# Performance work log

Measured on AMD Instinct MI355X. Metric: run time of the kernel, lower is better.

Reference implementation:

```python
import jax, jax.numpy as jnp
import numpy as np

DIM = 2048
INTER = 1408
N_EXPERTS = 16
TOP_K = 2
N_SHARED = 2
SHARED_INTER = N_SHARED * INTER  # 2816


def setup_inputs() -> dict:
    key = jax.random.key(0)
    ks = jax.random.split(key, 9)
    s = 0.02
    return {
        "x": jax.random.normal(ks[0], (4, 2048, DIM), dtype=jnp.float32),
        "gate_w": jax.random.normal(ks[1], (N_EXPERTS, DIM), dtype=jnp.float32) * s,
        "w1": jax.random.normal(ks[2], (N_EXPERTS, INTER, DIM), dtype=jnp.float32) * s,
        "w2": jax.random.normal(ks[3], (N_EXPERTS, DIM, INTER), dtype=jnp.float32) * s,
        "w3": jax.random.normal(ks[4], (N_EXPERTS, INTER, DIM), dtype=jnp.float32) * s,
        "sw1": jax.random.normal(ks[5], (SHARED_INTER, DIM), dtype=jnp.float32) * s,
        "sw2": jax.random.normal(ks[6], (DIM, SHARED_INTER), dtype=jnp.float32) * s,
        "sw3": jax.random.normal(ks[7], (SHARED_INTER, DIM), dtype=jnp.float32) * s,
    }


def _swiglu(t, wa, wb, wo):
    # t: [T, d_in]; wa, wb: [d_h, d_in]; wo: [d_out, d_h]
    h = jax.nn.silu(t @ wa.T) * (t @ wb.T)
    return h @ wo.T


def reference(x, gate_w, w1, w2, w3, sw1, sw2, sw3):
    shape = x.shape
    t = x.reshape(-1, DIM)                      # [T, dim]
    scores = jax.nn.softmax(t @ gate_w.T, axis=-1)  # [T, E]
    weights, indices = jax.lax.top_k(scores, TOP_K)  # [T, k] each

    y = jnp.zeros_like(t)
    # Small fixed loop over experts (structurally distinct weights).
    # Per-token combine weight for expert e: sum over top-k slots routed to e
    # (matches y[idx] += expert(x[idx]) * weights[idx, top]; zero weight for
    # unrouted tokens reproduces the counts[i]==0 skip exactly).
    for e in range(N_EXPERTS):
        w_e = jnp.sum(jnp.where(indices == e, weights, 0.0), axis=-1)  # [T]
        y = y + _swiglu(t, w1[e], w3[e], w2[e]) * w_e[:, None]

    z = _swiglu(t, sw1, sw3, sw2)               # shared experts MLP
    return (y + z).reshape(shape)
```

## Files before the change

### kernel.cpp

```cpp
#include <hip/hip_runtime.h>
#include <hip/hip_bf16.h>

#define DIM 2048
#define INTER 1408
#define NEXP 16
#define NTOK 8192
#define SINTER 2816

typedef __attribute__((ext_vector_type(8))) short bf16x8;
typedef __attribute__((ext_vector_type(4))) float f32x4;
typedef __attribute__((ext_vector_type(4))) unsigned short u16x4;
typedef __attribute__((ext_vector_type(8))) unsigned short u16x8;

#define VMCNT(n) asm volatile("s_waitcnt vmcnt(" #n ")" ::: "memory")
#define BARRIER() __builtin_amdgcn_s_barrier()

__device__ __forceinline__ unsigned short f2bf(float f) {
    union { float f; unsigned u; } a; a.f = f;
    unsigned r = a.u + 0x7fffu + ((a.u >> 16) & 1u);
    return (unsigned short)(r >> 16);
}
__device__ __forceinline__ float bf2f(unsigned short u) {
    union { unsigned u; float f; } a; a.u = ((unsigned)u) << 16; return a.f;
}

__device__ __forceinline__ void gload16(const void* g, void* lds) {
    __builtin_amdgcn_global_load_lds(
        (const __attribute__((address_space(1))) void*)g,
        (__attribute__((address_space(3))) void*)lds, 16, 0, 0);
}

__global__ __launch_bounds__(256) void cast_bf16(const float* __restrict__ s,
                                                 unsigned short* __restrict__ d,
                                                 long long n) {
    long long i = ((long long)blockIdx.x * 256 + threadIdx.x) * 8;
    if (i >= n) return;
    float4 a = *(const float4*)(s + i), b = *(const float4*)(s + i + 4);
    u16x8 o = { f2bf(a.x), f2bf(a.y), f2bf(a.z), f2bf(a.w),
                f2bf(b.x), f2bf(b.y), f2bf(b.z), f2bf(b.w) };
    *(u16x8*)(d + i) = o;
}

__global__ __launch_bounds__(256) void gate_topk(
    const float* __restrict__ x, const float* __restrict__ gw,
    unsigned short* __restrict__ xb,
    int* __restrict__ counts, int* __restrict__ toklist,
    int* __restrict__ se, int* __restrict__ sp, float* __restrict__ swt) {
    int wave = threadIdx.x >> 6;
    int lane = threadIdx.x & 63;
    int tok  = blockIdx.x * 4 + wave;
    const float* xr = x + (size_t)tok * DIM;
    unsigned short* xbr = xb + (size_t)tok * DIM;

    float part[NEXP];
#pragma unroll
    for (int e = 0; e < NEXP; ++e) part[e] = 0.f;
#pragma unroll
    for (int c = 0; c < DIM / 256; ++c) {
        float4 xv = *(const float4*)(xr + c * 256 + lane * 4);
        u16x4 xo = { f2bf(xv.x), f2bf(xv.y), f2bf(xv.z), f2bf(xv.w) };
        *(u16x4*)(xbr + c * 256 + lane * 4) = xo;
#pragma unroll
        for (int e = 0; e < NEXP; ++e) {
            float4 g = *(const float4*)(gw + e * DIM + c * 256 + lane * 4);
            part[e] += xv.x * g.x + xv.y * g.y + xv.z * g.z + xv.w * g.w;
        }
    }
#pragma unroll
    for (int e = 0; e < NEXP; ++e) {
        float v = part[e];
#pragma unroll
        for (int off = 32; off; off >>= 1) v += __shfl_xor(v, off);
        part[e] = v;
    }
    float mx = part[0];
#pragma unroll
    for (int e = 1; e < NEXP; ++e) mx = fmaxf(mx, part[e]);
    float Z = 0.f;
#pragma unroll
    for (int e = 0; e < NEXP; ++e) Z += expf(part[e] - mx);
    int i1 = 0; float m1 = part[0];
#pragma unroll
    for (int e = 1; e < NEXP; ++e) if (part[e] > m1) { m1 = part[e]; i1 = e; }
    int i2 = -1; float m2 = -1e30f;
#pragma unroll
    for (int e = 0; e < NEXP; ++e) if (e != i1 && part[e] > m2) { m2 = part[e]; i2 = e; }
    if (lane == 0) {
        float w1v = expf(m1 - mx) / Z;
        float w2v = expf(m2 - mx) / Z;
        int p1 = atomicAdd(&counts[i1], 1);
        toklist[i1 * NTOK + p1] = tok;
        int p2 = atomicAdd(&counts[i2], 1);
        toklist[i2 * NTOK + p2] = tok;
        se[2 * tok] = i1;  sp[2 * tok] = p1;  swt[2 * tok] = w1v;
        se[2 * tok + 1] = i2;  sp[2 * tok + 1] = p2;  swt[2 * tok + 1] = w2v;
    }
}

__global__ void prefix_k(const int* __restrict__ counts, int* __restrict__ base) {
    if (threadIdx.x == 0) {
        int acc = 0;
        for (int e = 0; e < NEXP; ++e) { base[e] = acc; acc += counts[e]; }
        base[16] = acc;
        base[17] = acc + NTOK;
    }
}

__global__ __launch_bounds__(512, 2) void gemm1(
    const unsigned short* __restrict__ xb,
    const unsigned short* __restrict__ w1b, const unsigned short* __restrict__ w3b,
    const unsigned short* __restrict__ sw1b, const unsigned short* __restrict__ sw3b,
    const int* __restrict__ counts, const int* __restrict__ base,
    const int* __restrict__ toklist, unsigned short* __restrict__ hbuf) {
    const int e   = blockIdx.z;
    const int cnt = (e < NEXP) ? counts[e] : NTOK;
    const int m0  = blockIdx.y * 256;
    if (m0 >= cnt) return;
    const int n0  = blockIdx.x * 128;
    const size_t woff = (size_t)((e < NEXP) ? e : e - NEXP) * INTER * DIM;
    const unsigned short* B1 = ((e < NEXP) ? w1b : sw1b) + woff;
    const unsigned short* B3 = ((e < NEXP) ? w3b : sw3b) + woff;
    const int hbase = base[e];
    const int* tl = toklist + e * NTOK;

    __shared__ __attribute__((aligned(16))) unsigned short As[2][16384];
    __shared__ __attribute__((aligned(16))) unsigned short B1s[2][8192];
    __shared__ __attribute__((aligned(16))) unsigned short B3s[2][8192];

    const int tid = threadIdx.x;
    const int w = tid >> 6, lu = tid & 63;
    const int wr = w >> 1, wc = w & 1;
    const int lr = lu & 15, hi = lu >> 4;

    const int srow = tid >> 3;
    const int sslot = tid & 7;
    const int cEl = ((sslot ^ (srow & 7)) * 8);

    const unsigned short* aSrc[4];
#pragma unroll
    for (int i = 0; i < 4; ++i) {
        int grow = m0 + 64 * i + srow;
        int t;
        if (e < NEXP) t = (grow < cnt) ? tl[grow] : 0;
        else          t = grow;
        aSrc[i] = xb + (size_t)t * DIM + cEl;
    }
    const unsigned short *b1Src[2], *b3Src[2];
#pragma unroll
    for (int i = 0; i < 2; ++i) {
        int r = n0 + 64 * i + srow;
        b1Src[i] = B1 + (size_t)r * DIM + cEl;
        b3Src[i] = B3 + (size_t)r * DIM + cEl;
    }

    int aoff[2][4], boff[2][4];
#pragma unroll
    for (int kk = 0; kk < 2; ++kk) {
#pragma unroll
        for (int m = 0; m < 4; ++m) {
            int R = wr * 64 + m * 16 + lr;
            aoff[kk][m] = R * 128 + (((kk * 4 + hi) ^ (lr & 7)) << 4);
        }
#pragma unroll
        for (int n = 0; n < 4; ++n) {
            int R = wc * 64 + n * 16 + lr;
            boff[kk][n] = R * 128 + (((kk * 4 + hi) ^ (lr & 7)) << 4);
        }
    }

    f32x4 acc1[4][4], acc3[4][4];
#pragma unroll
    for (int m = 0; m < 4; ++m)
#pragma unroll
        for (int n = 0; n < 4; ++n) {
            acc1[m][n] = (f32x4){0.f, 0.f, 0.f, 0.f};
            acc3[m][n] = (f32x4){0.f, 0.f, 0.f, 0.f};
        }

    const int H = DIM / 64;

    auto STAGE = [&](int hh) {
        int hb = hh & 1;
        int kc = hh * 64;
#pragma unroll
        for (int i = 0; i < 4; ++i)
            gload16(aSrc[i] + kc, &As[hb][i * 4096 + tid * 8]);
#pragma unroll
        for (int i = 0; i < 2; ++i) {
            gload16(b1Src[i] + kc, &B1s[hb][i * 4096 + tid * 8]);
            gload16(b3Src[i] + kc, &B3s[hb][i * 4096 + tid * 8]);
        }
    };

    STAGE(0);
    VMCNT(0);
    BARRIER();

    for (int h = 0; h < H; ++h) {
        const int hb = h & 1;
        const char* As_ = (const char*)&As[hb][0];
        const char* B1_ = (const char*)&B1s[hb][0];
        const char* B3_ = (const char*)&B3s[hb][0];
        bf16x8 af[4], b1f[4], b3f[4];
#pragma unroll
        for (int m = 0; m < 4; ++m) af[m] = *(const bf16x8*)(As_ + aoff[0][m]);
#pragma unroll
        for (int n = 0; n < 4; ++n) {
            b1f[n] = *(const bf16x8*)(B1_ + boff[0][n]);
            b3f[n] = *(const bf16x8*)(B3_ + boff[0][n]);
        }
        if (h + 1 < H) STAGE(h + 1);
        __builtin_amdgcn_s_setprio(1);
#pragma unroll
        for (int n = 0; n < 4; ++n)
#pragma unroll
            for (int m = 0; m < 4; ++m)
                acc1[m][n] = __builtin_amdgcn_mfma_f32_16x16x32_bf16(af[m], b1f[n], acc1[m][n], 0, 0, 0);
#pragma unroll
        for (int n = 0; n < 4; ++n)
#pragma unroll
            for (int m = 0; m < 4; ++m)
                acc3[m][n] = __builtin_amdgcn_mfma_f32_16x16x32_bf16(af[m], b3f[n], acc3[m][n], 0, 0, 0);
        __builtin_amdgcn_s_setprio(0);
#pragma unroll
        for (int m = 0; m < 4; ++m) af[m] = *(const bf16x8*)(As_ + aoff[1][m]);
#pragma unroll
        for (int n = 0; n < 4; ++n) {
            b1f[n] = *(const bf16x8*)(B1_ + boff[1][n]);
            b3f[n] = *(const bf16x8*)(B3_ + boff[1][n]);
        }
        __builtin_amdgcn_s_setprio(1);
#pragma unroll
        for (int n = 0; n < 4; ++n)
#pragma unroll
            for (int m = 0; m < 4; ++m)
                acc1[m][n] = __builtin_amdgcn_mfma_f32_16x16x32_bf16(af[m], b1f[n], acc1[m][n], 0, 0, 0);
#pragma unroll
        for (int n = 0; n < 4; ++n)
#pragma unroll
            for (int m = 0; m < 4; ++m)
                acc3[m][n] = __builtin_amdgcn_mfma_f32_16x16x32_bf16(af[m], b3f[n], acc3[m][n], 0, 0, 0);
        __builtin_amdgcn_s_setprio(0);
        VMCNT(0);
        BARRIER();
    }

#pragma unroll
    for (int m = 0; m < 4; ++m) {
#pragma unroll
        for (int i = 0; i < 4; ++i) {
            int row  = wr * 64 + m * 16 + hi * 4 + i;
            int grow = m0 + row;
            if (grow < cnt) {
                size_t ro = (size_t)(hbase + grow) * INTER;
#pragma unroll
                for (int n = 0; n < 4; ++n) {
                    int col = n0 + wc * 64 + n * 16 + lr;
                    float a = acc1[m][n][i];
                    float hv = a / (1.f + __expf(-a)) * acc3[m][n][i];
                    hbuf[ro + col] = f2bf(hv);
                }
            }
        }
    }
}

__global__ __launch_bounds__(512, 2) void gemm2(
    const unsigned short* __restrict__ hbuf,
    const unsigned short* __restrict__ w2b, const unsigned short* __restrict__ sw2b,
    const int* __restrict__ counts, const int* __restrict__ base,
    unsigned short* __restrict__ g2buf) {
    const int e   = blockIdx.z;
    const int cnt = (e < NEXP) ? counts[e] : NTOK;
    const int m0  = blockIdx.y * 256;
    if (m0 >= cnt) return;
    const int n0  = blockIdx.x * 256;
    const int hbase = base[e];
    const size_t bstride = (e < NEXP) ? INTER : SINTER;
    const unsigned short* Bb = (e < NEXP) ? w2b + (size_t)e * DIM * INTER
                                          : sw2b + (size_t)(e - NEXP) * INTER;

    __shared__ __attribute__((aligned(16))) unsigned short Ah[2][16384];
    __shared__ __attribute__((aligned(16))) unsigned short Bh[2][16384];

    const int tid = threadIdx.x;
    const int w = tid >> 6, lu = tid & 63;
    const int wr = w >> 2, wc = w & 3;
    const int lr = lu & 15, hi = lu >> 4;

    const int srow = tid >> 3;
    const int sslot = tid & 7;
    const int cEl = ((sslot ^ (srow & 7)) * 8);

    const unsigned short* aSrc[4];
#pragma unroll
    for (int i = 0; i < 4; ++i)
        aSrc[i] = hbuf + (size_t)(hbase + m0 + 64 * i + srow) * INTER + cEl;
    const unsigned short* bSrc[4];
#pragma unroll
    for (int i = 0; i < 4; ++i)
        bSrc[i] = Bb + (size_t)(n0 + 64 * i + srow) * bstride + cEl;

    int aoff[2][8], boff[2][4];
#pragma unroll
    for (int kk = 0; kk < 2; ++kk) {
#pragma unroll
        for (int m = 0; m < 8; ++m) {
            int R = wr * 128 + m * 16 + lr;
            aoff[kk][m] = R * 128 + (((kk * 4 + hi) ^ (lr & 7)) << 4);
        }
#pragma unroll
        for (int n = 0; n < 4; ++n) {
            int R = wc * 64 + n * 16 + lr;
            boff[kk][n] = R * 128 + (((kk * 4 + hi) ^ (lr & 7)) << 4);
        }
    }

    f32x4 acc[8][4];
#pragma unroll
    for (int m = 0; m < 8; ++m)
#pragma unroll
        for (int n = 0; n < 4; ++n) acc[m][n] = (f32x4){0.f, 0.f, 0.f, 0.f};

    const int H = INTER / 64;

    auto STAGE = [&](int hh) {
        int hb = hh & 1;
        int kc = hh * 64;
#pragma unroll
        for (int i = 0; i < 4; ++i)
            gload16(aSrc[i] + kc, &Ah[hb][i * 4096 + tid * 8]);
#pragma unroll
        for (int i = 0; i < 4; ++i)
            gload16(bSrc[i] + kc, &Bh[hb][i * 4096 + tid * 8]);
    };

    STAGE(0);
    VMCNT(0);
    BARRIER();

    for (int h = 0; h < H; ++h) {
        const int hb = h & 1;
        const char* A_ = (const char*)&Ah[hb][0];
        const char* B_ = (const char*)&Bh[hb][0];
        bf16x8 af[8], bf[4];
#pragma unroll
        for (int m = 0; m < 8; ++m) af[m] = *(const bf16x8*)(A_ + aoff[0][m]);
#pragma unroll
        for (int n = 0; n < 4; ++n) bf[n] = *(const bf16x8*)(B_ + boff[0][n]);
        if (h + 1 < H) STAGE(h + 1);
        __builtin_amdgcn_s_setprio(1);
#pragma unroll
        for (int n = 0; n < 4; ++n)
#pragma unroll
            for (int m = 0; m < 8; ++m)
                acc[m][n] = __builtin_amdgcn_mfma_f32_16x16x32_bf16(af[m], bf[n], acc[m][n], 0, 0, 0);
        __builtin_amdgcn_s_setprio(0);
#pragma unroll
        for (int m = 0; m < 8; ++m) af[m] = *(const bf16x8*)(A_ + aoff[1][m]);
#pragma unroll
        for (int n = 0; n < 4; ++n) bf[n] = *(const bf16x8*)(B_ + boff[1][n]);
        __builtin_amdgcn_s_setprio(1);
#pragma unroll
        for (int n = 0; n < 4; ++n)
#pragma unroll
            for (int m = 0; m < 8; ++m)
                acc[m][n] = __builtin_amdgcn_mfma_f32_16x16x32_bf16(af[m], bf[n], acc[m][n], 0, 0, 0);
        __builtin_amdgcn_s_setprio(0);
        VMCNT(0);
        BARRIER();
    }

#pragma unroll
    for (int m = 0; m < 8; ++m) {
#pragma unroll
        for (int i = 0; i < 4; ++i) {
            int row  = wr * 128 + m * 16 + hi * 4 + i;
            int grow = m0 + row;
            if (grow < cnt) {
                unsigned short* orow = g2buf + (size_t)(hbase + grow) * DIM + n0 + wc * 64 + lr;
#pragma unroll
                for (int n = 0; n < 4; ++n)
                    orow[n * 16] = f2bf(acc[m][n][i]);
            }
        }
    }
}

__global__ __launch_bounds__(256) void combine(
    const unsigned short* __restrict__ g2buf, const int* __restrict__ base,
    const int* __restrict__ se, const int* __restrict__ sp,
    const float* __restrict__ swt, float* __restrict__ out) {
    const int tok = blockIdx.x;
    const int c = threadIdx.x * 8;
    const int e0 = se[2 * tok], e1 = se[2 * tok + 1];
    const float w0 = swt[2 * tok], w1 = swt[2 * tok + 1];
    const size_t r0 = (size_t)(base[e0] + sp[2 * tok]) * DIM + c;
    const size_t r1 = (size_t)(base[e1] + sp[2 * tok + 1]) * DIM + c;
    const size_t r2 = (size_t)(2 * NTOK + tok) * DIM + c;
    const size_t r3 = (size_t)(3 * NTOK + tok) * DIM + c;
    u16x8 a = *(const u16x8*)(g2buf + r0);
    u16x8 b = *(const u16x8*)(g2buf + r1);
    u16x8 s0 = *(const u16x8*)(g2buf + r2);
    u16x8 s1 = *(const u16x8*)(g2buf + r3);
    float o[8];
#pragma unroll
    for (int j = 0; j < 8; ++j)
        o[j] = w0 * bf2f(a[j]) + w1 * bf2f(b[j]) + bf2f(s0[j]) + bf2f(s1[j]);
    float4* op = (float4*)(out + (size_t)tok * DIM + c);
    op[0] = make_float4(o[0], o[1], o[2], o[3]);
    op[1] = make_float4(o[4], o[5], o[6], o[7]);
}

extern "C" void kernel_launch(void* const* d_in, const int* in_sizes, int n_in,
                              void* d_out, int out_size, void* d_ws, size_t ws_size,
                              hipStream_t stream) {
    const float* x   = (const float*)d_in[0];
    const float* gw  = (const float*)d_in[1];
    const float* w1  = (const float*)d_in[2];
    const float* w2  = (const float*)d_in[3];
    const float* w3  = (const float*)d_in[4];
    const float* sw1 = (const float*)d_in[5];
    const float* sw2 = (const float*)d_in[6];
    const float* sw3 = (const float*)d_in[7];
    float* out = (float*)d_out;

    char* ws = (char*)d_ws;
    int*   counts  = (int*)ws;
    int*   basep   = (int*)(ws + 128);
    int*   toklist = (int*)(ws + 4096);
    int*   se      = (int*)(ws + 4096 + 524288);
    int*   sp      = (int*)(ws + 4096 + 524288 + 65536);
    float* swt     = (float*)(ws + 4096 + 524288 + 131072);

    unsigned short* hbuf = (unsigned short*)(ws + (2u << 20));

    const size_t hbytes = (size_t)4 * NTOK * INTER * 2;
    const size_t offx   = (2ull << 20) + hbytes;
    const size_t xbytes = (size_t)NTOK * DIM * 2;
    const size_t offw   = offx + xbytes;
    const size_t wB     = (size_t)NEXP * INTER * DIM * 2;
    const size_t swB    = (size_t)SINTER * DIM * 2;

    unsigned short* xb   = (unsigned short*)(ws + offx);
    unsigned short* w1b  = (unsigned short*)(ws + offw);
    unsigned short* w3b  = (unsigned short*)(ws + offw + wB);
    unsigned short* w2b  = (unsigned short*)(ws + offw + 2 * wB);
    unsigned short* sw1b = (unsigned short*)(ws + offw + 3 * wB);
    unsigned short* sw3b = (unsigned short*)(ws + offw + 3 * wB + swB);
    unsigned short* sw2b = (unsigned short*)(ws + offw + 3 * wB + 2 * swB);

    unsigned short* g2buf = (unsigned short*)(ws + offx);

    hipMemsetAsync(counts, 0, 64, stream);

    auto cast = [&](const float* s, unsigned short* d, long long n) {
        cast_bf16<<<(int)((n / 8 + 255) / 256), 256, 0, stream>>>(s, d, n);
    };
    cast(w1, w1b, (long long)NEXP * INTER * DIM);
    cast(w3, w3b, (long long)NEXP * INTER * DIM);
    cast(sw1, sw1b, (long long)SINTER * DIM);
    cast(sw3, sw3b, (long long)SINTER * DIM);
    cast(w2, w2b, (long long)NEXP * INTER * DIM);
    cast(sw2, sw2b, (long long)SINTER * DIM);

    gate_topk<<<NTOK / 4, 256, 0, stream>>>(x, gw, xb, counts, toklist, se, sp, swt);
    prefix_k<<<1, 64, 0, stream>>>(counts, basep);

    gemm1<<<dim3(INTER / 128, NTOK / 256, 18), 512, 0, stream>>>(
        xb, w1b, w3b, sw1b, sw3b, counts, basep, toklist, hbuf);

    gemm2<<<dim3(DIM / 256, NTOK / 256, 18), 512, 0, stream>>>(
        hbuf, w2b, sw2b, counts, basep, g2buf);

    combine<<<NTOK, 256, 0, stream>>>(g2buf, basep, se, sp, swt, out);
}
```

Before: 1.187 ms.

## Triple-buffer A tiles in expert GEMMs and fuse weight casts into one launch

Both grouped GEMMs now keep three LDS buffers for the gathered A tile and prefetch A two K-steps ahead (B one step ahead), issuing loads at the top of each iteration and waiting with a partial vmcnt. The aim is to hide the latency of the gathered activation loads behind more MFMA work. The six separate fp32-to-bf16 weight cast launches are merged into one kernel that picks the source by range, cutting launch overhead. The extra A buffer raises LDS use per block (gemm1 to 160KB with two blocks per CU requested), which may reduce occupancy. The partial vmcnt counts also have to match the number of loads actually issued.

```diff
diff --git a/kernel.cpp b/kernel.cpp
--- a/kernel.cpp
+++ b/kernel.cpp
@@ -30,15 +30,28 @@
         (__attribute__((address_space(3))) void*)lds, 16, 0, 0);
 }
 
-__global__ __launch_bounds__(256) void cast_bf16(const float* __restrict__ s,
-                                                 unsigned short* __restrict__ d,
-                                                 long long n) {
+__global__ __launch_bounds__(256) void cast_all(
+    const float* __restrict__ w1, const float* __restrict__ w3,
+    const float* __restrict__ w2, const float* __restrict__ sw1,
+    const float* __restrict__ sw3, const float* __restrict__ sw2,
+    unsigned short* __restrict__ w1b, unsigned short* __restrict__ w3b,
+    unsigned short* __restrict__ w2b, unsigned short* __restrict__ sw1b,
+    unsigned short* __restrict__ sw3b, unsigned short* __restrict__ sw2b) {
+    const long long NW = (long long)NEXP * INTER * DIM;
+    const long long NS = (long long)SINTER * DIM;
     long long i = ((long long)blockIdx.x * 256 + threadIdx.x) * 8;
-    if (i >= n) return;
-    float4 a = *(const float4*)(s + i), b = *(const float4*)(s + i + 4);
+    const float* s; unsigned short* d; long long off;
+    if      (i < NW)            { s = w1;  d = w1b;  off = i; }
+    else if (i < 2 * NW)        { s = w3;  d = w3b;  off = i - NW; }
+    else if (i < 3 * NW)        { s = w2;  d = w2b;  off = i - 2 * NW; }
+    else if (i < 3 * NW + NS)   { s = sw1; d = sw1b; off = i - 3 * NW; }
+    else if (i < 3 * NW + 2*NS) { s = sw3; d = sw3b; off = i - 3 * NW - NS; }
+    else if (i < 3 * NW + 3*NS) { s = sw2; d = sw2b; off = i - 3 * NW - 2 * NS; }
+    else return;
+    float4 a = *(const float4*)(s + off), b = *(const float4*)(s + off + 4);
     u16x8 o = { f2bf(a.x), f2bf(a.y), f2bf(a.z), f2bf(a.w),
                 f2bf(b.x), f2bf(b.y), f2bf(b.z), f2bf(b.w) };
-    *(u16x8*)(d + i) = o;
+    *(u16x8*)(d + off) = o;
 }
 
 __global__ __launch_bounds__(256) void gate_topk(
@@ -123,7 +136,7 @@
     const int hbase = base[e];
     const int* tl = toklist + e * NTOK;
 
-    __shared__ __attribute__((aligned(16))) unsigned short As[2][16384];
+    __shared__ __attribute__((aligned(16))) unsigned short As[3][16384];
     __shared__ __attribute__((aligned(16))) unsigned short B1s[2][8192];
     __shared__ __attribute__((aligned(16))) unsigned short B3s[2][8192];
 
@@ -179,28 +192,34 @@
 
     const int H = DIM / 64;
 
-    auto STAGE = [&](int hh) {
-        int hb = hh & 1;
+    auto STAGE_A = [&](int hh) {
+        int ab = hh % 3;
         int kc = hh * 64;
 #pragma unroll
         for (int i = 0; i < 4; ++i)
-            gload16(aSrc[i] + kc, &As[hb][i * 4096 + tid * 8]);
+            gload16(aSrc[i] + kc, &As[ab][i * 4096 + tid * 8]);
+    };
+    auto STAGE_B = [&](int hh) {
+        int bb = hh & 1;
+        int kc = hh * 64;
 #pragma unroll
         for (int i = 0; i < 2; ++i) {
-            gload16(b1Src[i] + kc, &B1s[hb][i * 4096 + tid * 8]);
-            gload16(b3Src[i] + kc, &B3s[hb][i * 4096 + tid * 8]);
+            gload16(b1Src[i] + kc, &B1s[bb][i * 4096 + tid * 8]);
+            gload16(b3Src[i] + kc, &B3s[bb][i * 4096 + tid * 8]);
         }
     };
 
-    STAGE(0);
-    VMCNT(0);
+    STAGE_A(0); STAGE_B(0); STAGE_A(1);
+    VMCNT(4);
     BARRIER();
 
     for (int h = 0; h < H; ++h) {
-        const int hb = h & 1;
-        const char* As_ = (const char*)&As[hb][0];
-        const char* B1_ = (const char*)&B1s[hb][0];
-        const char* B3_ = (const char*)&B3s[hb][0];
+        if (h + 2 < H)      { STAGE_B(h + 1); STAGE_A(h + 2); }
+        else if (h + 1 < H) { STAGE_B(h + 1); }
+        const int ab = h % 3, bb = h & 1;
+        const char* As_ = (const char*)&As[ab][0];
+        const char* B1_ = (const char*)&B1s[bb][0];
+        const char* B3_ = (const char*)&B3s[bb][0];
         bf16x8 af[4], b1f[4], b3f[4];
 #pragma unroll
         for (int m = 0; m < 4; ++m) af[m] = *(const bf16x8*)(As_ + aoff[0][m]);
@@ -209,7 +228,6 @@
             b1f[n] = *(const bf16x8*)(B1_ + boff[0][n]);
             b3f[n] = *(const bf16x8*)(B3_ + boff[0][n]);
         }
-        if (h + 1 < H) STAGE(h + 1);
         __builtin_amdgcn_s_setprio(1);
 #pragma unroll
         for (int n = 0; n < 4; ++n)
@@ -241,7 +259,7 @@
             for (int m = 0; m < 4; ++m)
                 acc3[m][n] = __builtin_amdgcn_mfma_f32_16x16x32_bf16(af[m], b3f[n], acc3[m][n], 0, 0, 0);
         __builtin_amdgcn_s_setprio(0);
-        VMCNT(0);
+        if (h + 2 < H) { VMCNT(4); } else { VMCNT(0); }
         BARRIER();
     }
 
@@ -280,7 +298,7 @@
     const unsigned short* Bb = (e < NEXP) ? w2b + (size_t)e * DIM * INTER
                                           : sw2b + (size_t)(e - NEXP) * INTER;
 
-    __shared__ __attribute__((aligned(16))) unsigned short Ah[2][16384];
+    __shared__ __attribute__((aligned(16))) unsigned short Ah[3][16384];
     __shared__ __attribute__((aligned(16))) unsigned short Bh[2][16384];
 
     const int tid = threadIdx.x;
@@ -324,31 +342,36 @@
 
     const int H = INTER / 64;
 
-    auto STAGE = [&](int hh) {
-        int hb = hh & 1;
+    auto STAGE_A = [&](int hh) {
+        int ab = hh % 3;
         int kc = hh * 64;
 #pragma unroll
         for (int i = 0; i < 4; ++i)
-            gload16(aSrc[i] + kc, &Ah[hb][i * 4096 + tid * 8]);
+            gload16(aSrc[i] + kc, &Ah[ab][i * 4096 + tid * 8]);
+    };
+    auto STAGE_B = [&](int hh) {
+        int bb = hh & 1;
+        int kc = hh * 64;
 #pragma unroll
         for (int i = 0; i < 4; ++i)
-            gload16(bSrc[i] + kc, &Bh[hb][i * 4096 + tid * 8]);
+            gload16(bSrc[i] + kc, &Bh[bb][i * 4096 + tid * 8]);
     };
 
-    STAGE(0);
-    VMCNT(0);
+    STAGE_A(0); STAGE_B(0); STAGE_A(1);
+    VMCNT(4);
     BARRIER();
 
     for (int h = 0; h < H; ++h) {
-        const int hb = h & 1;
-        const char* A_ = (const char*)&Ah[hb][0];
-        const char* B_ = (const char*)&Bh[hb][0];
+        if (h + 2 < H)      { STAGE_B(h + 1); STAGE_A(h + 2); }
+        else if (h + 1 < H) { STAGE_B(h + 1); }
+        const int ab = h % 3, bb = h & 1;
+        const char* A_ = (const char*)&Ah[ab][0];
+        const char* B_ = (const char*)&Bh[bb][0];
         bf16x8 af[8], bf[4];
 #pragma unroll
         for (int m = 0; m < 8; ++m) af[m] = *(const bf16x8*)(A_ + aoff[0][m]);
 #pragma unroll
         for (int n = 0; n < 4; ++n) bf[n] = *(const bf16x8*)(B_ + boff[0][n]);
-        if (h + 1 < H) STAGE(h + 1);
         __builtin_amdgcn_s_setprio(1);
 #pragma unroll
         for (int n = 0; n < 4; ++n)
@@ -367,7 +390,7 @@
             for (int m = 0; m < 8; ++m)
                 acc[m][n] = __builtin_amdgcn_mfma_f32_16x16x32_bf16(af[m], bf[n], acc[m][n], 0, 0, 0);
         __builtin_amdgcn_s_setprio(0);
-        VMCNT(0);
+        if (h + 2 < H) { VMCNT(4); } else { VMCNT(0); }
         BARRIER();
     }
 
@@ -454,15 +477,14 @@
 
     hipMemsetAsync(counts, 0, 64, stream);
 
-    auto cast = [&](const float* s, unsigned short* d, long long n) {
-        cast_bf16<<<(int)((n / 8 + 255) / 256), 256, 0, stream>>>(s, d, n);
-    };
-    cast(w1, w1b, (long long)NEXP * INTER * DIM);
-    cast(w3, w3b, (long long)NEXP * INTER * DIM);
-    cast(sw1, sw1b, (long long)SINTER * DIM);
-    cast(sw3, sw3b, (long long)SINTER * DIM);
-    cast(w2, w2b, (long long)NEXP * INTER * DIM);
-    cast(sw2, sw2b, (long long)SINTER * DIM);
+    {
+        const long long NW = (long long)NEXP * INTER * DIM;
+        const long long NS = (long long)SINTER * DIM;
+        long long total = 3 * NW + 3 * NS;
+        int grid = (int)((total / 8 + 255) / 256);
+        cast_all<<<grid, 256, 0, stream>>>(w1, w3, w2, sw1, sw3, sw2,
+                                           w1b, w3b, w2b, sw1b, sw3b, sw2b);
+    }
 
     gate_topk<<<NTOK / 4, 256, 0, stream>>>(x, gw, xb, counts, toklist, se, sp, swt);
     prefix_k<<<1, 64, 0, stream>>>(counts, basep);
```

After: 1.320 ms. +11.2%, slower.
